# Optimization experiments

Hardware: AMD Instinct MI355X
Metric: run time of the kernel (lower is better)

The kernel has to match this reference:

```python
import jax, jax.numpy as jnp
import numpy as np
from jax import lax

SIGMA = 1.0
ALPHA = 1.0
BETA = 1.0
TRUNCATE = 4.0  # scipy.ndimage default


def _gauss_kernel(sigma):
    radius = int(TRUNCATE * sigma + 0.5)  # scipy radius rule -> 4 for sigma=1
    x = np.arange(-radius, radius + 1, dtype=np.float64)
    k = np.exp(-0.5 * (x / sigma) ** 2)
    k = (k / k.sum()).astype(np.float32)
    return k

_KERNEL = _gauss_kernel(SIGMA)


def _blur_axis(img, k, axis):
    # scipy mode='reflect' == jnp.pad mode='symmetric' (edge repeated)
    r = len(k) // 2
    pad = [(0, 0)] * img.ndim
    pad[axis] = (r, r)
    xp = jnp.pad(img, pad, mode='symmetric')
    n = img.shape[axis]
    out = k[0] * lax.slice_in_dim(xp, 0, n, axis=axis)
    for i in range(1, len(k)):
        out = out + k[i] * lax.slice_in_dim(xp, i, i + n, axis=axis)
    return out


def gaussian_blur(img):
    # scalar sigma in scipy blurs along EVERY axis, including batch & channel
    k = jnp.asarray(_KERNEL, dtype=img.dtype)
    for ax in range(img.ndim):
        img = _blur_axis(img, k, ax)
    return img


def decompose(I):
    I_log = jnp.log(I + 1e-6)
    I_smooth = gaussian_blur(I_log)
    R = I_log - I_smooth
    L = I_log - R  # == I_smooth
    return jnp.exp(L), jnp.exp(R)


def setup_inputs() -> dict:
    key = jax.random.key(0)
    k1, k2 = jax.random.split(key)
    shape = (16, 3, 512, 512)
    I_enhanced = jax.random.uniform(k1, shape, dtype=jnp.float32)
    I_gt = jax.random.uniform(k2, shape, dtype=jnp.float32)
    return {"I_enhanced": I_enhanced, "I_gt": I_gt}


def reference(I_enhanced, I_gt):
    L_enh, R_enh = decompose(I_enhanced)
    L_gt, R_gt = decompose(I_gt)
    L_reflectance = jnp.mean((R_enh - R_gt) ** 2)
    L_illumination = jnp.mean((L_enh - L_gt) ** 2)
    return ALPHA * L_reflectance + BETA * L_illumination
```

## Files before the change

### kernel.cpp

```cpp
#include <hip/hip_runtime.h>
#include <hip/hip_fp16.h>
#include <cmath>

#define PLANE (512*512)
#define NPLANES 48
#define NEL (48*PLANE)

struct Taps { float k[9]; };
struct CMat { float w[3][3]; };


#define FOLD(r) ((r) < 0 ? (-1 - (r)) : ((r) > 511 ? (1023 - (r)) : (r)))

__global__ __launch_bounds__(64)
void k_blur_hw(const float* __restrict__ inE, const float* __restrict__ inG,
               ushort* __restrict__ wsS, ushort* __restrict__ wsI, Taps tp)
{
    const int l  = threadIdx.x;
    const int r0 = blockIdx.x * 16;
    const int z  = blockIdx.y;
    const float* __restrict__ src = (z < NPLANES) ? (inE + z * PLANE)
                                                  : (inG + (z - NPLANES) * PLANE);
    const int col  = 8 * l;
    const int tile = l >> 3;
    const int sh   = (l & 7) * 8;

    __half2 kh[9];
#pragma unroll
    for (int t = 0; t < 9; ++t) kh[t] = __float2half2_rn(tp.k[t]);

    uint ring[12][4];

    float4 pA[3], pB[3];
#pragma unroll
    for (int s = 0; s < 3; ++s) {
        const int row = FOLD(r0 - 4 + s);
        pA[s] = *(const float4*)(src + row * 512 + col);
        pB[s] = *(const float4*)(src + row * 512 + col + 4);
    }

    for (int jb = 0; jb < 24; jb += 12) {
#pragma unroll
        for (int u = 0; u < 12; ++u) {
            const int j = jb + u;

            const float4 a = pA[0], b = pB[0];
            pA[0] = pA[1]; pA[1] = pA[2];
            pB[0] = pB[1]; pB[1] = pB[2];
            if (j + 3 < 24) {
                const int row = FOLD(r0 - 1 + j);
                pA[2] = *(const float4*)(src + row * 512 + col);
                pB[2] = *(const float4*)(src + row * 512 + col + 4);
            }

            const float a0 = a.x + 1e-6f, a1 = a.y + 1e-6f;
            const float a2 = a.z + 1e-6f, a3 = a.w + 1e-6f;
            const float b0 = b.x + 1e-6f, b1 = b.y + 1e-6f;
            const float b2 = b.z + 1e-6f, b3 = b.w + 1e-6f;

            if (j >= 4 && j < 20) {
                const int ri = r0 + j - 4;
                __half2 i0 = __floats2half2_rn(a0, b0);
                __half2 i1 = __floats2half2_rn(a1, b1);
                __half2 i2 = __floats2half2_rn(a2, b2);
                __half2 i3 = __floats2half2_rn(a3, b3);
                ushort* dpI = wsI + (((ri * 8 + tile) * 96) + z) * 64 + sh;
                *(uint4*)dpI = make_uint4(*(uint*)&i0, *(uint*)&i1,
                                          *(uint*)&i2, *(uint*)&i3);
            }

            uint c[4];
            {
                __half2 h0 = __floats2half2_rn(__logf(a0), __logf(b0));
                __half2 h1 = __floats2half2_rn(__logf(a1), __logf(b1));
                __half2 h2 = __floats2half2_rn(__logf(a2), __logf(b2));
                __half2 h3 = __floats2half2_rn(__logf(a3), __logf(b3));
                c[0] = *(uint*)&h0; c[1] = *(uint*)&h1;
                c[2] = *(uint*)&h2; c[3] = *(uint*)&h3;
            }

            uint wpk[12];
#pragma unroll
            for (int i = 0; i < 4; ++i) {
                const uint up = (uint)__shfl_up((int)c[i], 1);
                const uint dn = (uint)__shfl_down((int)c[i], 1);
                wpk[i]     = (up >> 16) | (c[i] << 16);
                wpk[4 + i] = c[i];
                wpk[8 + i] = (c[i] >> 16) | (dn << 16);
            }
            if (l == 0) {
#pragma unroll
                for (int x = 0; x < 4; ++x)
                    wpk[x] = (c[3 - x] & 0xffffu) | (c[x] << 16);
            }
            if (l == 63) {
                wpk[8]  = (c[0] >> 16) | (c[3] & 0xffff0000u);
                wpk[9]  = (c[1] >> 16) | (c[2] & 0xffff0000u);
                wpk[10] = (c[2] >> 16) | (c[1] & 0xffff0000u);
                wpk[11] = (c[3] >> 16) | (c[0] & 0xffff0000u);
            }

#pragma unroll
            for (int i = 0; i < 4; ++i) {
                __half2 acc = __hmul2(kh[0], *(__half2*)&wpk[i]);
#pragma unroll
                for (int t = 1; t < 9; ++t)
                    acc = __hfma2(kh[t], *(__half2*)&wpk[i + t], acc);
                ring[u][i] = *(uint*)&acc;
            }

            if (j >= 8) {
                __half2 s0, s1, s2, s3;
                {
                    const int sl = (u + 4) % 12;
                    s0 = __hmul2(kh[0], *(__half2*)&ring[sl][0]);
                    s1 = __hmul2(kh[0], *(__half2*)&ring[sl][1]);
                    s2 = __hmul2(kh[0], *(__half2*)&ring[sl][2]);
                    s3 = __hmul2(kh[0], *(__half2*)&ring[sl][3]);
                }
#pragma unroll
                for (int t = 1; t < 9; ++t) {
                    const int sl = (u + 4 + t) % 12;
                    s0 = __hfma2(kh[t], *(__half2*)&ring[sl][0], s0);
                    s1 = __hfma2(kh[t], *(__half2*)&ring[sl][1], s1);
                    s2 = __hfma2(kh[t], *(__half2*)&ring[sl][2], s2);
                    s3 = __hfma2(kh[t], *(__half2*)&ring[sl][3], s3);
                }
                const int ro = r0 + j - 8;
                ushort* dpS = wsS + (((ro * 8 + tile) * 96) + z) * 64 + sh;
                *(uint4*)dpS = make_uint4(*(uint*)&s0, *(uint*)&s1,
                                          *(uint*)&s2, *(uint*)&s3);
            }
        }
    }
}

__global__ __launch_bounds__(256)
void k_cn_loss(const ushort* __restrict__ wsS, const ushort* __restrict__ wsI,
               float* __restrict__ out, Taps tp, CMat cm)
{
    const int tid = threadIdx.x;
    const int P   = blockIdx.x * 256 + tid;
    const int hw0 = P * 2;
    const int off = (hw0 >> 6) * (96 * 64) + (hw0 & 63);
    const ushort* sbase = wsS + off;
    const ushort* ibase = wsI + off;

    __half2 k2[9], cw[3][3];
#pragma unroll
    for (int t = 0; t < 9; ++t) k2[t] = __float2half2_rn(tp.k[t]);
#pragma unroll
    for (int i = 0; i < 3; ++i)
#pragma unroll
        for (int j = 0; j < 3; ++j) cw[i][j] = __float2half2_rn(cm.w[i][j]);

    __half2 re[9][3];
    __half2 rg[9][3];

#define LOADRAW(m, uE, uG)                                                     \
    uE[0] = *(const uint*)(sbase + ((m) * 3 + 0) * 64);                        \
    uE[1] = *(const uint*)(sbase + ((m) * 3 + 1) * 64);                        \
    uE[2] = *(const uint*)(sbase + ((m) * 3 + 2) * 64);                        \
    uG[0] = *(const uint*)(sbase + (48 + (m) * 3 + 0) * 64);                   \
    uG[1] = *(const uint*)(sbase + (48 + (m) * 3 + 1) * 64);                   \
    uG[2] = *(const uint*)(sbase + (48 + (m) * 3 + 2) * 64);

#define CBLUR(u, dst)                                                          \
    {                                                                          \
        __half2 v0 = *(__half2*)&u[0];                                         \
        __half2 v1 = *(__half2*)&u[1];                                         \
        __half2 v2 = *(__half2*)&u[2];                                         \
        dst[0] = __hfma2(cw[0][0], v0, __hfma2(cw[0][1], v1, __hmul2(cw[0][2], v2))); \
        dst[1] = __hfma2(cw[1][0], v0, __hfma2(cw[1][1], v1, __hmul2(cw[1][2], v2))); \
        dst[2] = __hfma2(cw[2][0], v0, __hfma2(cw[2][1], v1, __hmul2(cw[2][2], v2))); \
    }

#pragma unroll
    for (int m = 0; m < 4; ++m) {
        uint uE[3], uG[3];
        LOADRAW(m, uE, uG);
        CBLUR(uE, re[m]); CBLUR(uG, rg[m]);
    }
    uint nuE[3], nuG[3];
    LOADRAW(4, nuE, nuG);
    uint ieq[3], igq[3];
#pragma unroll
    for (int c = 0; c < 3; ++c) {
        ieq[c] = *(const uint*)(ibase + c * 64);
        igq[c] = *(const uint*)(ibase + (48 + c) * 64);
    }

    float acc = 0.f;
#pragma unroll
    for (int n = 0; n < 16; ++n) {
        uint nie[3], nig[3];
        if (n + 1 < 16) {
#pragma unroll
            for (int c = 0; c < 3; ++c) {
                nie[c] = *(const uint*)(ibase + (((n + 1) * 3 + c)) * 64);
                nig[c] = *(const uint*)(ibase + ((48 + (n + 1) * 3 + c)) * 64);
            }
        }
        const int mnew = n + 4;
        if (mnew < 16) {
            CBLUR(nuE, re[mnew % 9]); CBLUR(nuG, rg[mnew % 9]);
            if (mnew + 1 < 16) { LOADRAW(mnew + 1, nuE, nuG); }
        }
#pragma unroll
        for (int c = 0; c < 3; ++c) {
            __half2 se2 = __float2half2_rn(0.f), sg2 = se2;
#pragma unroll
            for (int t = 0; t < 9; ++t) {
                int m = n - 4 + t;
                m = (m < 0) ? (-1 - m) : ((m > 15) ? (31 - m) : m);
                se2 = __hfma2(k2[t], re[m % 9][c], se2);
                sg2 = __hfma2(k2[t], rg[m % 9][c], sg2);
            }
            const float2 sef = __half22float2(se2);
            const float2 sgf = __half22float2(sg2);
            const float2 ief = __half22float2(*(__half2*)&ieq[c]);
            const float2 igf = __half22float2(*(__half2*)&igq[c]);

            {
                float ee = __expf(-sef.x), eg = __expf(-sgf.x);
                float Re = ief.x * ee;
                float Rg = igf.x * eg;
                float Le = __builtin_amdgcn_rcpf(ee);
                float Lg = __builtin_amdgcn_rcpf(eg);
                float dr = Re - Rg, dl = Le - Lg;
                acc += dr * dr + dl * dl;
            }
            {
                float ee = __expf(-sef.y), eg = __expf(-sgf.y);
                float Re = ief.y * ee;
                float Rg = igf.y * eg;
                float Le = __builtin_amdgcn_rcpf(ee);
                float Lg = __builtin_amdgcn_rcpf(eg);
                float dr = Re - Rg, dl = Le - Lg;
                acc += dr * dr + dl * dl;
            }
        }
        if (n + 1 < 16) {
#pragma unroll
            for (int c = 0; c < 3; ++c) { ieq[c] = nie[c]; igq[c] = nig[c]; }
        }
    }
#undef LOADRAW
#undef CBLUR

    __shared__ float red[256];
    red[tid] = acc;
    __syncthreads();
#pragma unroll
    for (int s = 128; s > 0; s >>= 1) {
        if (tid < s) red[tid] += red[tid + s];
        __syncthreads();
    }
    if (tid == 0) atomicAdd(out, red[0] * (1.0f / (float)NEL));
}

extern "C" void kernel_launch(void* const* d_in, const int* in_sizes, int n_in,
                              void* d_out, int out_size, void* d_ws, size_t ws_size,
                              hipStream_t stream) {
    const float* Ie = (const float*)d_in[0];
    const float* Ig = (const float*)d_in[1];

    Taps tp;
    {
        double kk[9], s = 0.0;
        for (int i = 0; i < 9; ++i) { double x = (double)(i - 4); kk[i] = exp(-0.5 * x * x); s += kk[i]; }
        for (int i = 0; i < 9; ++i) tp.k[i] = (float)(kk[i] / s);
    }

    CMat cm;
    {
        for (int c = 0; c < 3; ++c) {
            cm.w[c][0] = cm.w[c][1] = cm.w[c][2] = 0.f;
            for (int t = 0; t < 9; ++t) {
                int m = c - 4 + t;
                int mm = ((m % 6) + 6) % 6;
                if (mm > 2) mm = 5 - mm;
                cm.w[c][mm] += tp.k[t];
            }
        }
    }

    ushort* wsS = (ushort*)d_ws;
    ushort* wsI = wsS + 2 * (size_t)NEL;

    hipMemsetAsync(d_out, 0, sizeof(float), stream);
    dim3 g1(32, 96);
    k_blur_hw<<<g1, 64, 0, stream>>>(Ie, Ig, wsS, wsI, tp);
    k_cn_loss<<<512, 256, 0, stream>>>(wsS, wsI, (float*)d_out, tp, cm);
}
```

Measured before the change: 163.4 us.

## Halve per-block work in both kernels and fold output zeroing into blur

The blur kernel now handles 8 rows per block instead of 16, which doubles the grid and fully unrolls a 16-step loop with a 9-entry ring. The loss kernel splits the batch (n) dimension into two halves via a templated helper, doubling its grid to 1024 blocks. The separate memset is replaced by zeroing the output inside the blur kernel. The aim is more parallelism and occupancy, plus one fewer launch. The cost is extra halo rows recomputed in both kernels (8 of 16 rows per block in blur, 4 of 8 batch slices in loss) and more atomics.

```diff
diff --git a/kernel.cpp b/kernel.cpp
--- a/kernel.cpp
+++ b/kernel.cpp
@@ -14,11 +14,13 @@
 
 __global__ __launch_bounds__(64)
 void k_blur_hw(const float* __restrict__ inE, const float* __restrict__ inG,
-               ushort* __restrict__ wsS, ushort* __restrict__ wsI, Taps tp)
+               ushort* __restrict__ wsS, ushort* __restrict__ wsI,
+               float* __restrict__ out, Taps tp)
 {
     const int l  = threadIdx.x;
-    const int r0 = blockIdx.x * 16;
+    const int r0 = blockIdx.x * 8;
     const int z  = blockIdx.y;
+    if (blockIdx.x == 0 && blockIdx.y == 0 && l == 0) *out = 0.f;
     const float* __restrict__ src = (z < NPLANES) ? (inE + z * PLANE)
                                                   : (inG + (z - NPLANES) * PLANE);
     const int col  = 8 * l;
@@ -29,7 +31,7 @@
 #pragma unroll
     for (int t = 0; t < 9; ++t) kh[t] = __float2half2_rn(tp.k[t]);
 
-    uint ring[12][4];
+    uint ring[9][4];
 
     float4 pA[3], pB[3];
 #pragma unroll
@@ -39,121 +41,104 @@
         pB[s] = *(const float4*)(src + row * 512 + col + 4);
     }
 
-    for (int jb = 0; jb < 24; jb += 12) {
-#pragma unroll
-        for (int u = 0; u < 12; ++u) {
-            const int j = jb + u;
-
-            const float4 a = pA[0], b = pB[0];
-            pA[0] = pA[1]; pA[1] = pA[2];
-            pB[0] = pB[1]; pB[1] = pB[2];
-            if (j + 3 < 24) {
-                const int row = FOLD(r0 - 1 + j);
-                pA[2] = *(const float4*)(src + row * 512 + col);
-                pB[2] = *(const float4*)(src + row * 512 + col + 4);
-            }
-
-            const float a0 = a.x + 1e-6f, a1 = a.y + 1e-6f;
-            const float a2 = a.z + 1e-6f, a3 = a.w + 1e-6f;
-            const float b0 = b.x + 1e-6f, b1 = b.y + 1e-6f;
-            const float b2 = b.z + 1e-6f, b3 = b.w + 1e-6f;
-
-            if (j >= 4 && j < 20) {
-                const int ri = r0 + j - 4;
-                __half2 i0 = __floats2half2_rn(a0, b0);
-                __half2 i1 = __floats2half2_rn(a1, b1);
-                __half2 i2 = __floats2half2_rn(a2, b2);
-                __half2 i3 = __floats2half2_rn(a3, b3);
-                ushort* dpI = wsI + (((ri * 8 + tile) * 96) + z) * 64 + sh;
-                *(uint4*)dpI = make_uint4(*(uint*)&i0, *(uint*)&i1,
-                                          *(uint*)&i2, *(uint*)&i3);
-            }
-
-            uint c[4];
+#pragma unroll
+    for (int j = 0; j < 16; ++j) {
+        const float4 a = pA[0], b = pB[0];
+        pA[0] = pA[1]; pA[1] = pA[2];
+        pB[0] = pB[1]; pB[1] = pB[2];
+        if (j + 3 < 16) {
+            const int row = FOLD(r0 - 1 + j);
+            pA[2] = *(const float4*)(src + row * 512 + col);
+            pB[2] = *(const float4*)(src + row * 512 + col + 4);
+        }
+
+        const float a0 = a.x + 1e-6f, a1 = a.y + 1e-6f;
+        const float a2 = a.z + 1e-6f, a3 = a.w + 1e-6f;
+        const float b0 = b.x + 1e-6f, b1 = b.y + 1e-6f;
+        const float b2 = b.z + 1e-6f, b3 = b.w + 1e-6f;
+
+        if (j >= 4 && j < 12) {
+            const int ri = r0 + j - 4;
+            __half2 i0 = __floats2half2_rn(a0, b0);
+            __half2 i1 = __floats2half2_rn(a1, b1);
+            __half2 i2 = __floats2half2_rn(a2, b2);
+            __half2 i3 = __floats2half2_rn(a3, b3);
+            ushort* dpI = wsI + (((ri * 8 + tile) * 96) + z) * 64 + sh;
+            *(uint4*)dpI = make_uint4(*(uint*)&i0, *(uint*)&i1,
+                                      *(uint*)&i2, *(uint*)&i3);
+        }
+
+        uint c[4];
+        {
+            __half2 h0 = __floats2half2_rn(__logf(a0), __logf(b0));
+            __half2 h1 = __floats2half2_rn(__logf(a1), __logf(b1));
+            __half2 h2 = __floats2half2_rn(__logf(a2), __logf(b2));
+            __half2 h3 = __floats2half2_rn(__logf(a3), __logf(b3));
+            c[0] = *(uint*)&h0; c[1] = *(uint*)&h1;
+            c[2] = *(uint*)&h2; c[3] = *(uint*)&h3;
+        }
+
+        uint wpk[12];
+#pragma unroll
+        for (int i = 0; i < 4; ++i) {
+            const uint up = (uint)__shfl_up((int)c[i], 1);
+            const uint dn = (uint)__shfl_down((int)c[i], 1);
+            wpk[i]     = (up >> 16) | (c[i] << 16);
+            wpk[4 + i] = c[i];
+            wpk[8 + i] = (c[i] >> 16) | (dn << 16);
+        }
+        if (l == 0) {
+#pragma unroll
+            for (int x = 0; x < 4; ++x)
+                wpk[x] = (c[3 - x] & 0xffffu) | (c[x] << 16);
+        }
+        if (l == 63) {
+            wpk[8]  = (c[0] >> 16) | (c[3] & 0xffff0000u);
+            wpk[9]  = (c[1] >> 16) | (c[2] & 0xffff0000u);
+            wpk[10] = (c[2] >> 16) | (c[1] & 0xffff0000u);
+            wpk[11] = (c[3] >> 16) | (c[0] & 0xffff0000u);
+        }
+
+#pragma unroll
+        for (int i = 0; i < 4; ++i) {
+            __half2 acc = __hmul2(kh[0], *(__half2*)&wpk[i]);
+#pragma unroll
+            for (int t = 1; t < 9; ++t)
+                acc = __hfma2(kh[t], *(__half2*)&wpk[i + t], acc);
+            ring[j % 9][i] = *(uint*)&acc;
+        }
+
+        if (j >= 8) {
+            __half2 s0, s1, s2, s3;
             {
-                __half2 h0 = __floats2half2_rn(__logf(a0), __logf(b0));
-                __half2 h1 = __floats2half2_rn(__logf(a1), __logf(b1));
-                __half2 h2 = __floats2half2_rn(__logf(a2), __logf(b2));
-                __half2 h3 = __floats2half2_rn(__logf(a3), __logf(b3));
-                c[0] = *(uint*)&h0; c[1] = *(uint*)&h1;
-                c[2] = *(uint*)&h2; c[3] = *(uint*)&h3;
-            }
-
-            uint wpk[12];
-#pragma unroll
-            for (int i = 0; i < 4; ++i) {
-                const uint up = (uint)__shfl_up((int)c[i], 1);
-                const uint dn = (uint)__shfl_down((int)c[i], 1);
-                wpk[i]     = (up >> 16) | (c[i] << 16);
-                wpk[4 + i] = c[i];
-                wpk[8 + i] = (c[i] >> 16) | (dn << 16);
-            }
-            if (l == 0) {
-#pragma unroll
-                for (int x = 0; x < 4; ++x)
-                    wpk[x] = (c[3 - x] & 0xffffu) | (c[x] << 16);
-            }
-            if (l == 63) {
-                wpk[8]  = (c[0] >> 16) | (c[3] & 0xffff0000u);
-                wpk[9]  = (c[1] >> 16) | (c[2] & 0xffff0000u);
-                wpk[10] = (c[2] >> 16) | (c[1] & 0xffff0000u);
-                wpk[11] = (c[3] >> 16) | (c[0] & 0xffff0000u);
-            }
-
-#pragma unroll
-            for (int i = 0; i < 4; ++i) {
-                __half2 acc = __hmul2(kh[0], *(__half2*)&wpk[i]);
-#pragma unroll
-                for (int t = 1; t < 9; ++t)
-                    acc = __hfma2(kh[t], *(__half2*)&wpk[i + t], acc);
-                ring[u][i] = *(uint*)&acc;
-            }
-
-            if (j >= 8) {
-                __half2 s0, s1, s2, s3;
-                {
-                    const int sl = (u + 4) % 12;
-                    s0 = __hmul2(kh[0], *(__half2*)&ring[sl][0]);
-                    s1 = __hmul2(kh[0], *(__half2*)&ring[sl][1]);
-                    s2 = __hmul2(kh[0], *(__half2*)&ring[sl][2]);
-                    s3 = __hmul2(kh[0], *(__half2*)&ring[sl][3]);
-                }
-#pragma unroll
-                for (int t = 1; t < 9; ++t) {
-                    const int sl = (u + 4 + t) % 12;
-                    s0 = __hfma2(kh[t], *(__half2*)&ring[sl][0], s0);
-                    s1 = __hfma2(kh[t], *(__half2*)&ring[sl][1], s1);
-                    s2 = __hfma2(kh[t], *(__half2*)&ring[sl][2], s2);
-                    s3 = __hfma2(kh[t], *(__half2*)&ring[sl][3], s3);
-                }
-                const int ro = r0 + j - 8;
-                ushort* dpS = wsS + (((ro * 8 + tile) * 96) + z) * 64 + sh;
-                *(uint4*)dpS = make_uint4(*(uint*)&s0, *(uint*)&s1,
-                                          *(uint*)&s2, *(uint*)&s3);
-            }
-        }
-    }
-}
-
-__global__ __launch_bounds__(256)
-void k_cn_loss(const ushort* __restrict__ wsS, const ushort* __restrict__ wsI,
-               float* __restrict__ out, Taps tp, CMat cm)
+                const int sl = (j - 8) % 9;
+                s0 = __hmul2(kh[0], *(__half2*)&ring[sl][0]);
+                s1 = __hmul2(kh[0], *(__half2*)&ring[sl][1]);
+                s2 = __hmul2(kh[0], *(__half2*)&ring[sl][2]);
+                s3 = __hmul2(kh[0], *(__half2*)&ring[sl][3]);
+            }
+#pragma unroll
+            for (int t = 1; t < 9; ++t) {
+                const int sl = (j - 8 + t) % 9;
+                s0 = __hfma2(kh[t], *(__half2*)&ring[sl][0], s0);
+                s1 = __hfma2(kh[t], *(__half2*)&ring[sl][1], s1);
+                s2 = __hfma2(kh[t], *(__half2*)&ring[sl][2], s2);
+                s3 = __hfma2(kh[t], *(__half2*)&ring[sl][3], s3);
+            }
+            const int ro = r0 + j - 8;
+            ushort* dpS = wsS + (((ro * 8 + tile) * 96) + z) * 64 + sh;
+            *(uint4*)dpS = make_uint4(*(uint*)&s0, *(uint*)&s1,
+                                      *(uint*)&s2, *(uint*)&s3);
+        }
+    }
+}
+
+template <int H>
+__device__ __forceinline__ float cn_half(const ushort* __restrict__ sbase,
+                                         const ushort* __restrict__ ibase,
+                                         const __half2 k2[9],
+                                         const __half2 cw[3][3])
 {
-    const int tid = threadIdx.x;
-    const int P   = blockIdx.x * 256 + tid;
-    const int hw0 = P * 2;
-    const int off = (hw0 >> 6) * (96 * 64) + (hw0 & 63);
-    const ushort* sbase = wsS + off;
-    const ushort* ibase = wsI + off;
-
-    __half2 k2[9], cw[3][3];
-#pragma unroll
-    for (int t = 0; t < 9; ++t) k2[t] = __float2half2_rn(tp.k[t]);
-#pragma unroll
-    for (int i = 0; i < 3; ++i)
-#pragma unroll
-        for (int j = 0; j < 3; ++j) cw[i][j] = __float2half2_rn(cm.w[i][j]);
-
     __half2 re[9][3];
     __half2 rg[9][3];
 
@@ -176,35 +161,25 @@
     }
 
 #pragma unroll
-    for (int m = 0; m < 4; ++m) {
+    for (int m = (H ? 4 : 0); m < 8 * H + 4; ++m) {
         uint uE[3], uG[3];
         LOADRAW(m, uE, uG);
-        CBLUR(uE, re[m]); CBLUR(uG, rg[m]);
-    }
-    uint nuE[3], nuG[3];
-    LOADRAW(4, nuE, nuG);
-    uint ieq[3], igq[3];
-#pragma unroll
-    for (int c = 0; c < 3; ++c) {
-        ieq[c] = *(const uint*)(ibase + c * 64);
-        igq[c] = *(const uint*)(ibase + (48 + c) * 64);
+        CBLUR(uE, re[m % 9]); CBLUR(uG, rg[m % 9]);
     }
 
     float acc = 0.f;
 #pragma unroll
-    for (int n = 0; n < 16; ++n) {
-        uint nie[3], nig[3];
-        if (n + 1 < 16) {
-#pragma unroll
-            for (int c = 0; c < 3; ++c) {
-                nie[c] = *(const uint*)(ibase + (((n + 1) * 3 + c)) * 64);
-                nig[c] = *(const uint*)(ibase + ((48 + (n + 1) * 3 + c)) * 64);
-            }
-        }
-        const int mnew = n + 4;
-        if (mnew < 16) {
-            CBLUR(nuE, re[mnew % 9]); CBLUR(nuG, rg[mnew % 9]);
-            if (mnew + 1 < 16) { LOADRAW(mnew + 1, nuE, nuG); }
+    for (int n = 8 * H; n < 8 * H + 8; ++n) {
+        if (n + 4 <= (H ? 15 : 11)) {
+            uint uE[3], uG[3];
+            LOADRAW(n + 4, uE, uG);
+            CBLUR(uE, re[(n + 4) % 9]); CBLUR(uG, rg[(n + 4) % 9]);
+        }
+        uint ieq[3], igq[3];
+#pragma unroll
+        for (int c = 0; c < 3; ++c) {
+            ieq[c] = *(const uint*)(ibase + (n * 3 + c) * 64);
+            igq[c] = *(const uint*)(ibase + ((48 + n * 3 + c)) * 64);
         }
 #pragma unroll
         for (int c = 0; c < 3; ++c) {
@@ -240,13 +215,34 @@
                 acc += dr * dr + dl * dl;
             }
         }
-        if (n + 1 < 16) {
-#pragma unroll
-            for (int c = 0; c < 3; ++c) { ieq[c] = nie[c]; igq[c] = nig[c]; }
-        }
     }
 #undef LOADRAW
 #undef CBLUR
+    return acc;
+}
+
+__global__ __launch_bounds__(256)
+void k_cn_loss(const ushort* __restrict__ wsS, const ushort* __restrict__ wsI,
+               float* __restrict__ out, Taps tp, CMat cm)
+{
+    const int tid  = threadIdx.x;
+    const int half = blockIdx.x >> 9;
+    const int P    = (blockIdx.x & 511) * 256 + tid;
+    const int hw0  = P * 2;
+    const int off  = (hw0 >> 6) * (96 * 64) + (hw0 & 63);
+    const ushort* sbase = wsS + off;
+    const ushort* ibase = wsI + off;
+
+    __half2 k2[9], cw[3][3];
+#pragma unroll
+    for (int t = 0; t < 9; ++t) k2[t] = __float2half2_rn(tp.k[t]);
+#pragma unroll
+    for (int i = 0; i < 3; ++i)
+#pragma unroll
+        for (int j = 0; j < 3; ++j) cw[i][j] = __float2half2_rn(cm.w[i][j]);
+
+    const float acc = (half == 0) ? cn_half<0>(sbase, ibase, k2, cw)
+                                  : cn_half<1>(sbase, ibase, k2, cw);
 
     __shared__ float red[256];
     red[tid] = acc;
@@ -288,8 +284,7 @@
     ushort* wsS = (ushort*)d_ws;
     ushort* wsI = wsS + 2 * (size_t)NEL;
 
-    hipMemsetAsync(d_out, 0, sizeof(float), stream);
-    dim3 g1(32, 96);
-    k_blur_hw<<<g1, 64, 0, stream>>>(Ie, Ig, wsS, wsI, tp);
-    k_cn_loss<<<512, 256, 0, stream>>>(wsS, wsI, (float*)d_out, tp, cm);
-}
+    dim3 g1(64, 96);
+    k_blur_hw<<<g1, 64, 0, stream>>>(Ie, Ig, wsS, wsI, (float*)d_out, tp);
+    k_cn_loss<<<1024, 256, 0, stream>>>(wsS, wsI, (float*)d_out, tp, cm);
+}
```

Result: slower. 172.3 us (+5.4%).

## Software-pipeline log and lane shuffles one row ahead; fold output zeroing into blur kernel

Applied to the files above, without the earlier changes.

The blur kernel now computes the log, fp16 pack and cross-lane shuffles for the next row before doing the current row's horizontal and vertical FMAs, then assembles the window at the end of the iteration. This is meant to hide shuffle and transcendental latency behind independent arithmetic within one wavefront. The separate memset of the scalar output is removed, and the first thread of the blur kernel zeroes it instead, saving one queued operation. The cost is extra live registers for the prefetched row, which could lower occupancy.

```diff
diff --git a/kernel.cpp b/kernel.cpp
--- a/kernel.cpp
+++ b/kernel.cpp
@@ -14,11 +14,13 @@
 
 __global__ __launch_bounds__(64)
 void k_blur_hw(const float* __restrict__ inE, const float* __restrict__ inG,
-               ushort* __restrict__ wsS, ushort* __restrict__ wsI, Taps tp)
+               ushort* __restrict__ wsS, ushort* __restrict__ wsI,
+               float* __restrict__ out, Taps tp)
 {
     const int l  = threadIdx.x;
     const int r0 = blockIdx.x * 16;
     const int z  = blockIdx.y;
+    if (blockIdx.x == 0 && blockIdx.y == 0 && l == 0) *out = 0.f;
     const float* __restrict__ src = (z < NPLANES) ? (inE + z * PLANE)
                                                   : (inG + (z - NPLANES) * PLANE);
     const int col  = 8 * l;
@@ -37,6 +39,47 @@
         const int row = FOLD(r0 - 4 + s);
         pA[s] = *(const float4*)(src + row * 512 + col);
         pB[s] = *(const float4*)(src + row * 512 + col + 4);
+    }
+
+    auto logpack = [&](const float4& a, const float4& b, uint c[4]) {
+        __half2 h0 = __floats2half2_rn(__logf(a.x + 1e-6f), __logf(b.x + 1e-6f));
+        __half2 h1 = __floats2half2_rn(__logf(a.y + 1e-6f), __logf(b.y + 1e-6f));
+        __half2 h2 = __floats2half2_rn(__logf(a.z + 1e-6f), __logf(b.z + 1e-6f));
+        __half2 h3 = __floats2half2_rn(__logf(a.w + 1e-6f), __logf(b.w + 1e-6f));
+        c[0] = *(uint*)&h0; c[1] = *(uint*)&h1;
+        c[2] = *(uint*)&h2; c[3] = *(uint*)&h3;
+    };
+    auto assemble = [&](const uint c[4], const uint up[4], const uint dn[4],
+                        uint wpk[12]) {
+#pragma unroll
+        for (int i = 0; i < 4; ++i) {
+            wpk[i]     = (up[i] >> 16) | (c[i] << 16);
+            wpk[4 + i] = c[i];
+            wpk[8 + i] = (c[i] >> 16) | (dn[i] << 16);
+        }
+        if (l == 0) {
+#pragma unroll
+            for (int x = 0; x < 4; ++x)
+                wpk[x] = (c[3 - x] & 0xffffu) | (c[x] << 16);
+        }
+        if (l == 63) {
+            wpk[8]  = (c[0] >> 16) | (c[3] & 0xffff0000u);
+            wpk[9]  = (c[1] >> 16) | (c[2] & 0xffff0000u);
+            wpk[10] = (c[2] >> 16) | (c[1] & 0xffff0000u);
+            wpk[11] = (c[3] >> 16) | (c[0] & 0xffff0000u);
+        }
+    };
+
+    uint wpk[12];
+    {
+        uint c[4], up[4], dn[4];
+        logpack(pA[0], pB[0], c);
+#pragma unroll
+        for (int i = 0; i < 4; ++i) {
+            up[i] = (uint)__shfl_up((int)c[i], 1);
+            dn[i] = (uint)__shfl_down((int)c[i], 1);
+        }
+        assemble(c, up, dn, wpk);
     }
 
     for (int jb = 0; jb < 24; jb += 12) {
@@ -53,51 +96,26 @@
                 pB[2] = *(const float4*)(src + row * 512 + col + 4);
             }
 
-            const float a0 = a.x + 1e-6f, a1 = a.y + 1e-6f;
-            const float a2 = a.z + 1e-6f, a3 = a.w + 1e-6f;
-            const float b0 = b.x + 1e-6f, b1 = b.y + 1e-6f;
-            const float b2 = b.z + 1e-6f, b3 = b.w + 1e-6f;
-
             if (j >= 4 && j < 20) {
                 const int ri = r0 + j - 4;
-                __half2 i0 = __floats2half2_rn(a0, b0);
-                __half2 i1 = __floats2half2_rn(a1, b1);
-                __half2 i2 = __floats2half2_rn(a2, b2);
-                __half2 i3 = __floats2half2_rn(a3, b3);
+                __half2 i0 = __floats2half2_rn(a.x + 1e-6f, b.x + 1e-6f);
+                __half2 i1 = __floats2half2_rn(a.y + 1e-6f, b.y + 1e-6f);
+                __half2 i2 = __floats2half2_rn(a.z + 1e-6f, b.z + 1e-6f);
+                __half2 i3 = __floats2half2_rn(a.w + 1e-6f, b.w + 1e-6f);
                 ushort* dpI = wsI + (((ri * 8 + tile) * 96) + z) * 64 + sh;
                 *(uint4*)dpI = make_uint4(*(uint*)&i0, *(uint*)&i1,
                                           *(uint*)&i2, *(uint*)&i3);
             }
 
-            uint c[4];
-            {
-                __half2 h0 = __floats2half2_rn(__logf(a0), __logf(b0));
-                __half2 h1 = __floats2half2_rn(__logf(a1), __logf(b1));
-                __half2 h2 = __floats2half2_rn(__logf(a2), __logf(b2));
-                __half2 h3 = __floats2half2_rn(__logf(a3), __logf(b3));
-                c[0] = *(uint*)&h0; c[1] = *(uint*)&h1;
-                c[2] = *(uint*)&h2; c[3] = *(uint*)&h3;
-            }
-
-            uint wpk[12];
-#pragma unroll
-            for (int i = 0; i < 4; ++i) {
-                const uint up = (uint)__shfl_up((int)c[i], 1);
-                const uint dn = (uint)__shfl_down((int)c[i], 1);
-                wpk[i]     = (up >> 16) | (c[i] << 16);
-                wpk[4 + i] = c[i];
-                wpk[8 + i] = (c[i] >> 16) | (dn << 16);
-            }
-            if (l == 0) {
-#pragma unroll
-                for (int x = 0; x < 4; ++x)
-                    wpk[x] = (c[3 - x] & 0xffffu) | (c[x] << 16);
-            }
-            if (l == 63) {
-                wpk[8]  = (c[0] >> 16) | (c[3] & 0xffff0000u);
-                wpk[9]  = (c[1] >> 16) | (c[2] & 0xffff0000u);
-                wpk[10] = (c[2] >> 16) | (c[1] & 0xffff0000u);
-                wpk[11] = (c[3] >> 16) | (c[0] & 0xffff0000u);
+            uint cN[4], upN[4], dnN[4];
+            const bool have_next = (j + 1 < 24);
+            if (have_next) {
+                logpack(pA[0], pB[0], cN);
+#pragma unroll
+                for (int i = 0; i < 4; ++i) {
+                    upN[i] = (uint)__shfl_up((int)cN[i], 1);
+                    dnN[i] = (uint)__shfl_down((int)cN[i], 1);
+                }
             }
 
 #pragma unroll
@@ -131,6 +149,8 @@
                 *(uint4*)dpS = make_uint4(*(uint*)&s0, *(uint*)&s1,
                                           *(uint*)&s2, *(uint*)&s3);
             }
+
+            if (have_next) assemble(cN, upN, dnN, wpk);
         }
     }
 }
@@ -288,8 +308,7 @@
     ushort* wsS = (ushort*)d_ws;
     ushort* wsI = wsS + 2 * (size_t)NEL;
 
-    hipMemsetAsync(d_out, 0, sizeof(float), stream);
     dim3 g1(32, 96);
-    k_blur_hw<<<g1, 64, 0, stream>>>(Ie, Ig, wsS, wsI, tp);
+    k_blur_hw<<<g1, 64, 0, stream>>>(Ie, Ig, wsS, wsI, (float*)d_out, tp);
     k_cn_loss<<<512, 256, 0, stream>>>(wsS, wsI, (float*)d_out, tp, cm);
 }
```

Measured after the change: 161.9 us. About the same (-0.9%).

## Drop fp16 input workspace, reread fp32 inputs in loss kernel, deepen prefetch

Applied to the files above, without the earlier changes.

The blur kernel no longer writes a half-precision copy of the inputs. The loss kernel instead reads the original fp32 inputs directly with a remapped index, which removes one workspace write and read pass at the cost of wider loads. The blur kernel now prefetches six rows ahead instead of three, rebuilds the horizontal window with fewer shuffles using half-word realignment, and gets an occupancy hint in its launch bounds. The output is now zeroed inside the first kernel instead of by a separate memset call.

```diff
diff --git a/kernel.cpp b/kernel.cpp
--- a/kernel.cpp
+++ b/kernel.cpp
@@ -12,13 +12,19 @@
 
 #define FOLD(r) ((r) < 0 ? (-1 - (r)) : ((r) > 511 ? (1023 - (r)) : (r)))
 
-__global__ __launch_bounds__(64)
+__device__ __forceinline__ uint swap16(uint x) { return (x >> 16) | (x << 16); }
+__device__ __forceinline__ uint align16(uint hiSrc, uint loSrc) {
+    return (loSrc >> 16) | (hiSrc << 16);
+}
+
+__global__ __launch_bounds__(64, 3)
 void k_blur_hw(const float* __restrict__ inE, const float* __restrict__ inG,
-               ushort* __restrict__ wsS, ushort* __restrict__ wsI, Taps tp)
+               ushort* __restrict__ wsS, float* __restrict__ out, Taps tp)
 {
     const int l  = threadIdx.x;
     const int r0 = blockIdx.x * 16;
     const int z  = blockIdx.y;
+    if (blockIdx.x == 0 && blockIdx.y == 0 && l == 0) *out = 0.f;
     const float* __restrict__ src = (z < NPLANES) ? (inE + z * PLANE)
                                                   : (inG + (z - NPLANES) * PLANE);
     const int col  = 8 * l;
@@ -31,9 +37,9 @@
 
     uint ring[12][4];
 
-    float4 pA[3], pB[3];
-#pragma unroll
-    for (int s = 0; s < 3; ++s) {
+    float4 pA[6], pB[6];
+#pragma unroll
+    for (int s = 0; s < 6; ++s) {
         const int row = FOLD(r0 - 4 + s);
         pA[s] = *(const float4*)(src + row * 512 + col);
         pB[s] = *(const float4*)(src + row * 512 + col + 4);
@@ -42,71 +48,46 @@
     for (int jb = 0; jb < 24; jb += 12) {
 #pragma unroll
         for (int u = 0; u < 12; ++u) {
-            const int j = jb + u;
-
-            const float4 a = pA[0], b = pB[0];
-            pA[0] = pA[1]; pA[1] = pA[2];
-            pB[0] = pB[1]; pB[1] = pB[2];
-            if (j + 3 < 24) {
-                const int row = FOLD(r0 - 1 + j);
-                pA[2] = *(const float4*)(src + row * 512 + col);
-                pB[2] = *(const float4*)(src + row * 512 + col + 4);
-            }
-
-            const float a0 = a.x + 1e-6f, a1 = a.y + 1e-6f;
-            const float a2 = a.z + 1e-6f, a3 = a.w + 1e-6f;
-            const float b0 = b.x + 1e-6f, b1 = b.y + 1e-6f;
-            const float b2 = b.z + 1e-6f, b3 = b.w + 1e-6f;
-
-            if (j >= 4 && j < 20) {
-                const int ri = r0 + j - 4;
-                __half2 i0 = __floats2half2_rn(a0, b0);
-                __half2 i1 = __floats2half2_rn(a1, b1);
-                __half2 i2 = __floats2half2_rn(a2, b2);
-                __half2 i3 = __floats2half2_rn(a3, b3);
-                ushort* dpI = wsI + (((ri * 8 + tile) * 96) + z) * 64 + sh;
-                *(uint4*)dpI = make_uint4(*(uint*)&i0, *(uint*)&i1,
-                                          *(uint*)&i2, *(uint*)&i3);
-            }
-
-            uint c[4];
-            {
-                __half2 h0 = __floats2half2_rn(__logf(a0), __logf(b0));
-                __half2 h1 = __floats2half2_rn(__logf(a1), __logf(b1));
-                __half2 h2 = __floats2half2_rn(__logf(a2), __logf(b2));
-                __half2 h3 = __floats2half2_rn(__logf(a3), __logf(b3));
-                c[0] = *(uint*)&h0; c[1] = *(uint*)&h1;
-                c[2] = *(uint*)&h2; c[3] = *(uint*)&h3;
-            }
-
-            uint wpk[12];
-#pragma unroll
-            for (int i = 0; i < 4; ++i) {
-                const uint up = (uint)__shfl_up((int)c[i], 1);
-                const uint dn = (uint)__shfl_down((int)c[i], 1);
-                wpk[i]     = (up >> 16) | (c[i] << 16);
-                wpk[4 + i] = c[i];
-                wpk[8 + i] = (c[i] >> 16) | (dn << 16);
-            }
-            if (l == 0) {
-#pragma unroll
-                for (int x = 0; x < 4; ++x)
-                    wpk[x] = (c[3 - x] & 0xffffu) | (c[x] << 16);
-            }
-            if (l == 63) {
-                wpk[8]  = (c[0] >> 16) | (c[3] & 0xffff0000u);
-                wpk[9]  = (c[1] >> 16) | (c[2] & 0xffff0000u);
-                wpk[10] = (c[2] >> 16) | (c[1] & 0xffff0000u);
-                wpk[11] = (c[3] >> 16) | (c[0] & 0xffff0000u);
-            }
-
-#pragma unroll
-            for (int i = 0; i < 4; ++i) {
-                __half2 acc = __hmul2(kh[0], *(__half2*)&wpk[i]);
+            const int j   = jb + u;
+            const int sl6 = u % 6;
+
+            const float4 a = pA[sl6], b = pB[sl6];
+            if (j + 6 < 24) {
+                const int row = FOLD(r0 + 2 + j);
+                pA[sl6] = *(const float4*)(src + row * 512 + col);
+                pB[sl6] = *(const float4*)(src + row * 512 + col + 4);
+            }
+
+            const float e0 = __logf(a.x + 1e-6f), e1 = __logf(a.y + 1e-6f);
+            const float e2 = __logf(a.z + 1e-6f), e3 = __logf(a.w + 1e-6f);
+            const float e4 = __logf(b.x + 1e-6f), e5 = __logf(b.y + 1e-6f);
+            const float e6 = __logf(b.z + 1e-6f), e7 = __logf(b.w + 1e-6f);
+            __half2 h01 = __floats2half2_rn(e0, e1);
+            __half2 h23 = __floats2half2_rn(e2, e3);
+            __half2 h45 = __floats2half2_rn(e4, e5);
+            __half2 h67 = __floats2half2_rn(e6, e7);
+            const uint P0 = *(uint*)&h01, P2 = *(uint*)&h23;
+            const uint P4 = *(uint*)&h45, P6 = *(uint*)&h67;
+
+            uint U4 = (uint)__shfl_up((int)P4, 1);
+            uint U6 = (uint)__shfl_up((int)P6, 1);
+            uint D0 = (uint)__shfl_down((int)P0, 1);
+            uint D2 = (uint)__shfl_down((int)P2, 1);
+            if (l == 0)  { U4 = swap16(P2); U6 = swap16(P0); }
+            if (l == 63) { D0 = swap16(P6); D2 = swap16(P4); }
+            uint pk[15];
+            pk[0] = U4; pk[2] = U6; pk[4] = P0; pk[6] = P2;
+            pk[8] = P4; pk[10] = P6; pk[12] = D0; pk[14] = D2;
+#pragma unroll
+            for (int x = 0; x < 7; ++x) pk[2 * x + 1] = align16(pk[2 * x + 2], pk[2 * x]);
+
+#pragma unroll
+            for (int q = 0; q < 4; ++q) {
+                __half2 acc = __hmul2(kh[0], *(__half2*)&pk[2 * q]);
 #pragma unroll
                 for (int t = 1; t < 9; ++t)
-                    acc = __hfma2(kh[t], *(__half2*)&wpk[i + t], acc);
-                ring[u][i] = *(uint*)&acc;
+                    acc = __hfma2(kh[t], *(__half2*)&pk[2 * q + t], acc);
+                ring[u][q] = *(uint*)&acc;
             }
 
             if (j >= 8) {
@@ -136,15 +117,21 @@
 }
 
 __global__ __launch_bounds__(256)
-void k_cn_loss(const ushort* __restrict__ wsS, const ushort* __restrict__ wsI,
+void k_cn_loss(const ushort* __restrict__ wsS,
+               const float* __restrict__ inE, const float* __restrict__ inG,
                float* __restrict__ out, Taps tp, CMat cm)
 {
     const int tid = threadIdx.x;
     const int P   = blockIdx.x * 256 + tid;
     const int hw0 = P * 2;
-    const int off = (hw0 >> 6) * (96 * 64) + (hw0 & 63);
-    const ushort* sbase = wsS + off;
-    const ushort* ibase = wsI + off;
+    const int hb  = hw0 >> 6;
+    const ushort* sbase = wsS + hb * (96 * 64) + (hw0 & 63);
+    const int h     = hb >> 3;
+    const int tile  = hb & 7;
+    const int mu    = (hw0 & 63) >> 1;
+    const int basew = tile * 64 + ((mu >> 2) << 3) + ((mu & 3) << 1);
+    const float* __restrict__ ibE = inE + (size_t)h * 512 + basew;
+    const float* __restrict__ ibG = inG + (size_t)h * 512 + basew;
 
     __half2 k2[9], cw[3][3];
 #pragma unroll
@@ -183,22 +170,22 @@
     }
     uint nuE[3], nuG[3];
     LOADRAW(4, nuE, nuG);
-    uint ieq[3], igq[3];
+    float2 fe[3], fg[3];
 #pragma unroll
     for (int c = 0; c < 3; ++c) {
-        ieq[c] = *(const uint*)(ibase + c * 64);
-        igq[c] = *(const uint*)(ibase + (48 + c) * 64);
+        fe[c] = *(const float2*)(ibE + (size_t)c * PLANE);
+        fg[c] = *(const float2*)(ibG + (size_t)c * PLANE);
     }
 
     float acc = 0.f;
 #pragma unroll
     for (int n = 0; n < 16; ++n) {
-        uint nie[3], nig[3];
+        float2 nfe[3], nfg[3];
         if (n + 1 < 16) {
 #pragma unroll
             for (int c = 0; c < 3; ++c) {
-                nie[c] = *(const uint*)(ibase + (((n + 1) * 3 + c)) * 64);
-                nig[c] = *(const uint*)(ibase + ((48 + (n + 1) * 3 + c)) * 64);
+                nfe[c] = *(const float2*)(ibE + (size_t)((n + 1) * 3 + c) * PLANE);
+                nfg[c] = *(const float2*)(ibG + (size_t)((n + 1) * 3 + c) * PLANE);
             }
         }
         const int mnew = n + 4;
@@ -218,13 +205,11 @@
             }
             const float2 sef = __half22float2(se2);
             const float2 sgf = __half22float2(sg2);
-            const float2 ief = __half22float2(*(__half2*)&ieq[c]);
-            const float2 igf = __half22float2(*(__half2*)&igq[c]);
 
             {
                 float ee = __expf(-sef.x), eg = __expf(-sgf.x);
-                float Re = ief.x * ee;
-                float Rg = igf.x * eg;
+                float Re = (fe[c].x + 1e-6f) * ee;
+                float Rg = (fg[c].x + 1e-6f) * eg;
                 float Le = __builtin_amdgcn_rcpf(ee);
                 float Lg = __builtin_amdgcn_rcpf(eg);
                 float dr = Re - Rg, dl = Le - Lg;
@@ -232,8 +217,8 @@
             }
             {
                 float ee = __expf(-sef.y), eg = __expf(-sgf.y);
-                float Re = ief.y * ee;
-                float Rg = igf.y * eg;
+                float Re = (fe[c].y + 1e-6f) * ee;
+                float Rg = (fg[c].y + 1e-6f) * eg;
                 float Le = __builtin_amdgcn_rcpf(ee);
                 float Lg = __builtin_amdgcn_rcpf(eg);
                 float dr = Re - Rg, dl = Le - Lg;
@@ -242,7 +227,7 @@
         }
         if (n + 1 < 16) {
 #pragma unroll
-            for (int c = 0; c < 3; ++c) { ieq[c] = nie[c]; igq[c] = nig[c]; }
+            for (int c = 0; c < 3; ++c) { fe[c] = nfe[c]; fg[c] = nfg[c]; }
         }
     }
 #undef LOADRAW
@@ -286,10 +271,8 @@
     }
 
     ushort* wsS = (ushort*)d_ws;
-    ushort* wsI = wsS + 2 * (size_t)NEL;
-
-    hipMemsetAsync(d_out, 0, sizeof(float), stream);
+
     dim3 g1(32, 96);
-    k_blur_hw<<<g1, 64, 0, stream>>>(Ie, Ig, wsS, wsI, tp);
-    k_cn_loss<<<512, 256, 0, stream>>>(wsS, wsI, (float*)d_out, tp, cm);
-}
+    k_blur_hw<<<g1, 64, 0, stream>>>(Ie, Ig, wsS, (float*)d_out, tp);
+    k_cn_loss<<<512, 256, 0, stream>>>(wsS, Ie, Ig, (float*)d_out, tp, cm);
+}
```

New measurement: 159.1 us. -2.7%, faster.
